# Kernel tuning notes

Hardware: AMD Instinct MI355X
Metric: run time of the kernel (lower is better)

The kernel has to match this reference:

```python
import jax, jax.numpy as jnp
import numpy as np

NUM_FEAT = 10

def _flatten(x):
    # [B,T,C,H,W] -> [B,C,T*H*W]
    B, T, C, H, W = x.shape
    return jnp.transpose(x, (0, 2, 1, 3, 4)).reshape(B, C, T * H * W)

def _conv1x1(w, b, x):
    # pointwise Conv1d: w [F,C], b [F], x [B,C,N] -> [B,F,N]
    return jnp.einsum('fc,bcn->bfn', w, x) + b[None, :, None]

def setup_inputs() -> dict:
    key = jax.random.key(0)
    ks = jax.random.split(key, 9)
    B, T, C, H, W = 1, 5, 64, 32, 32
    F = NUM_FEAT
    return {
        'input1': jax.random.normal(ks[0], (B, T, C, H, W), jnp.float32),
        'input2': jax.random.normal(ks[1], (B, T, C, H, W), jnp.float32),
        'act_weights': jax.random.uniform(ks[2], (3,), jnp.float32),
        'conv1_w': jax.random.normal(ks[3], (F, C), jnp.float32) * 0.05,
        'conv1_b': jnp.zeros((F,), jnp.float32),
        'conv2_w': jax.random.normal(ks[4], (F, C), jnp.float32) * 0.05,
        'conv2_b': jnp.zeros((F,), jnp.float32),
        'g3_w': jax.random.normal(ks[5], (F, C), jnp.float32) * 0.05,
        'g3_b': jnp.zeros((F,), jnp.float32),
    }

def reference(input1, input2, act_weights, conv1_w, conv1_b, conv2_w, conv2_b, g3_w, g3_b):
    B, T, C, H, W = input1.shape
    F = conv1_w.shape[0]
    x1 = _flatten(input1)                    # [B,C,N]
    x2 = _flatten(input2)                    # [B,C,N]
    q = _conv1x1(conv1_w, conv1_b, x1)       # [B,F,N]
    k = _conv1x1(conv2_w, conv2_b, x2)       # [B,F,N]
    v = _conv1x1(g3_w, g3_b, x1)             # [B,F,N]
    scores = jnp.einsum('bfn,bfm->bnm', q, k)  # [B,N,N] (same math, computed once)

    def branch(act_scores):
        o = jnp.einsum('bnm,bfm->bnf', act_scores, v)      # [B,N,F]
        o = o.reshape(B, T, H, W, F)
        return jnp.transpose(o, (0, 1, 4, 2, 3))           # [B,T,F,H,W]

    out = act_weights[0] * branch(jax.nn.relu(scores))
    out = out + act_weights[1] * branch(jax.nn.sigmoid(scores))
    # NOTE: original code scales the softmax branch by act_weights[0] (bug kept faithfully)
    out = out + act_weights[0] * branch(jax.nn.softmax(scores, axis=1))
    return out
```

## Files before the change

### kernel.cpp

```cpp
#include <hip/hip_runtime.h>

#define N_TOK   5120
#define C_IN    64
#define F_OUT   10
#define FP      12

#define DTILE   40
#define MTILE   40

__global__ __launch_bounds__(256) void qkv_kernel(
    const float* __restrict__ x1, const float* __restrict__ x2,
    const float* __restrict__ w1, const float* __restrict__ b1,
    const float* __restrict__ w2, const float* __restrict__ b2,
    const float* __restrict__ w3, const float* __restrict__ b3,
    float* __restrict__ Q, float* __restrict__ K, float* __restrict__ V)
{
    int arr = blockIdx.x / 200;
    int rem = blockIdx.x - arr * 200;
    int f   = rem / 20;
    int nbk = rem - f * 20;
    int n   = nbk * 256 + threadIdx.x;
    int t = n >> 10, p = n & 1023;

    const float* x    = (arr == 1) ? x2 : x1;
    const float* w    = (arr == 0) ? w1 : (arr == 1) ? w2 : w3;
    const float* bias = (arr == 0) ? b1 : (arr == 1) ? b2 : b3;
    float*       dst  = (arr == 0) ? Q  : (arr == 1) ? K  : V;

    const float* xp = x + t * (C_IN * 1024) + p;
    const float* wr = w + f * C_IN;

    float4 wv[16];
#pragma unroll
    for (int i = 0; i < 16; ++i) wv[i] = ((const float4*)wr)[i];

    float acc = 0.f;
#pragma unroll
    for (int i = 0; i < 16; ++i) {
        acc = fmaf(wv[i].x, xp[(4 * i + 0) * 1024], acc);
        acc = fmaf(wv[i].y, xp[(4 * i + 1) * 1024], acc);
        acc = fmaf(wv[i].z, xp[(4 * i + 2) * 1024], acc);
        acc = fmaf(wv[i].w, xp[(4 * i + 3) * 1024], acc);
    }
    dst[n * FP + f] = acc + bias[f];
}

__global__ __launch_bounds__(256) void denom_kernel(
    const float* __restrict__ Q, const float* __restrict__ K,
    float* __restrict__ dpart, int nclen)
{
    int mTile = blockIdx.x % 5;
    int nc    = blockIdx.x / 5;
    int tid   = threadIdx.x;
    int m0 = mTile * 1024 + tid;

    float kk[4][10];
#pragma unroll
    for (int c = 0; c < 4; ++c) {
        const float* kp = K + (m0 + c * 256) * FP;
        float4 a = ((const float4*)kp)[0];
        float4 b = ((const float4*)kp)[1];
        float2 e = ((const float2*)kp)[4];
        kk[c][0]=a.x; kk[c][1]=a.y; kk[c][2]=a.z; kk[c][3]=a.w;
        kk[c][4]=b.x; kk[c][5]=b.y; kk[c][6]=b.z; kk[c][7]=b.w;
        kk[c][8]=e.x; kk[c][9]=e.y;
    }

    __shared__ __align__(16) float sq[DTILE * FP];

    float d[4] = {0.f, 0.f, 0.f, 0.f};
    int n0 = nc * nclen;
    for (int base = n0; base < n0 + nclen; base += DTILE) {
        __syncthreads();
        if (tid < DTILE * FP / 4)
            ((float4*)sq)[tid] = ((const float4*)(Q + base * FP))[tid];
        __syncthreads();
#pragma unroll 2
        for (int j = 0; j < DTILE; ++j) {
            const float4* qp = (const float4*)(sq + j * FP);
            float4 qa = qp[0], qb = qp[1], qc = qp[2];
            float qq[10] = {qa.x, qa.y, qa.z, qa.w, qb.x, qb.y, qb.z, qb.w,
                            qc.x, qc.y};
#pragma unroll
            for (int c = 0; c < 4; ++c) {
                float s = 0.f;
#pragma unroll
                for (int f = 0; f < F_OUT; ++f) s = fmaf(qq[f], kk[c][f], s);
                d[c] += __expf(fminf(s, 60.f));
            }
        }
    }
#pragma unroll
    for (int c = 0; c < 4; ++c) dpart[nc * N_TOK + m0 + c * 256] = d[c];
}

__global__ __launch_bounds__(256) void invw_kernel(
    const float* __restrict__ dpart, const float* __restrict__ aw,
    float* __restrict__ K, int nchunks)
{
    int m = blockIdx.x * 256 + threadIdx.x;
    float d = 0.f;
#pragma unroll 8
    for (int c = 0; c < nchunks; ++c) d += dpart[c * N_TOK + m];
    K[m * FP + 10] = aw[0] / d;
}

__global__ __launch_bounds__(256) void main_kernel(
    const float* __restrict__ Q, const float* __restrict__ K,
    const float* __restrict__ V, const float* __restrict__ aw,
    float* __restrict__ opart, int mclen)
{
    int nTile = blockIdx.x % 4;
    int mc    = blockIdx.x / 4;
    int tid   = threadIdx.x;
    int nb = nTile * 1280 + tid;
    float w0 = aw[0], w1v = aw[1];

    float q[5][10];
#pragma unroll
    for (int r = 0; r < 5; ++r) {
        const float* qp = Q + (nb + r * 256) * FP;
        float4 a = ((const float4*)qp)[0];
        float4 b = ((const float4*)qp)[1];
        float2 e = ((const float2*)qp)[4];
        q[r][0]=a.x; q[r][1]=a.y; q[r][2]=a.z; q[r][3]=a.w;
        q[r][4]=b.x; q[r][5]=b.y; q[r][6]=b.z; q[r][7]=b.w;
        q[r][8]=e.x; q[r][9]=e.y;
    }

    float acc[5][F_OUT];
#pragma unroll
    for (int r = 0; r < 5; ++r)
#pragma unroll
        for (int f = 0; f < F_OUT; ++f) acc[r][f] = 0.f;

    __shared__ __align__(16) float sk[MTILE * FP];
    __shared__ __align__(16) float sv[MTILE * FP];

    int mstart = mc * mclen;
    for (int mbase = mstart; mbase < mstart + mclen; mbase += MTILE) {
        __syncthreads();
        if (tid < 120)
            ((float4*)sk)[tid] = ((const float4*)(K + mbase * FP))[tid];
        else if (tid < 240)
            ((float4*)sv)[tid - 120] = ((const float4*)(V + mbase * FP))[tid - 120];
        __syncthreads();

#pragma unroll 2
        for (int j = 0; j < MTILE; ++j) {
            const float4* kp = (const float4*)(sk + j * FP);
            float4 ka = kp[0], kb = kp[1], kc = kp[2];
            float kk[10] = {ka.x, ka.y, ka.z, ka.w, kb.x, kb.y, kb.z, kb.w,
                            kc.x, kc.y};
            float iw = kc.z;
            const float4* vp = (const float4*)(sv + j * FP);
            float4 va = vp[0], vb = vp[1], vc = vp[2];
            float vv[10] = {va.x, va.y, va.z, va.w, vb.x, vb.y, vb.z, vb.w,
                            vc.x, vc.y};

#pragma unroll
            for (int r = 0; r < 5; ++r) {
                float s = 0.f;
#pragma unroll
                for (int f = 0; f < F_OUT; ++f) s = fmaf(q[r][f], kk[f], s);
                float rl = fmaxf(s, 0.f);
                float e  = __expf(fminf(s, 60.f));
                float sg = e * __builtin_amdgcn_rcpf(1.f + e);
                float cf = fmaf(e, iw, fmaf(w1v, sg, w0 * rl));
#pragma unroll
                for (int f = 0; f < F_OUT; ++f) acc[r][f] = fmaf(cf, vv[f], acc[r][f]);
            }
        }
    }

#pragma unroll
    for (int r = 0; r < 5; ++r) {
        float2* o = (float2*)(opart + (size_t)(mc * N_TOK + nb + r * 256) * F_OUT);
#pragma unroll
        for (int f = 0; f < 5; ++f)
            o[f] = make_float2(acc[r][2 * f], acc[r][2 * f + 1]);
    }
}

__global__ __launch_bounds__(256) void reduce_kernel(
    const float* __restrict__ opart, float* __restrict__ out, int mchunks)
{
    int idx = blockIdx.x * 256 + threadIdx.x;
    float s = 0.f;
#pragma unroll 16
    for (int c = 0; c < mchunks; ++c) s += opart[c * (N_TOK * F_OUT) + idx];
    unsigned un = (unsigned)idx / 10u;
    int n = (int)un;
    int f = idx - n * 10;
    int t = n >> 10, p = n & 1023;
    out[((t * F_OUT + f) << 10) + p] = s;
}

extern "C" void kernel_launch(void* const* d_in, const int* in_sizes, int n_in,
                              void* d_out, int out_size, void* d_ws, size_t ws_size,
                              hipStream_t stream)
{
    const float* in1 = (const float*)d_in[0];
    const float* in2 = (const float*)d_in[1];
    const float* aw  = (const float*)d_in[2];
    const float* w1  = (const float*)d_in[3];
    const float* b1  = (const float*)d_in[4];
    const float* w2  = (const float*)d_in[5];
    const float* b2  = (const float*)d_in[6];
    const float* w3  = (const float*)d_in[7];
    const float* b3  = (const float*)d_in[8];
    float* out = (float*)d_out;

    int nchunks, mchunks;
    if (ws_size >= (size_t)32 << 20) { nchunks = 128; mchunks = 128; }
    else                             { nchunks = 32;  mchunks = 32;  }
    int nclen = N_TOK / nchunks;
    int mclen = N_TOK / mchunks;

    float* ws    = (float*)d_ws;
    float* Q     = ws;
    float* K     = Q + N_TOK * FP;
    float* V     = K + N_TOK * FP;
    float* dpart = V + N_TOK * FP;
    float* opart = dpart + nchunks * N_TOK;

    qkv_kernel<<<600, 256, 0, stream>>>(in1, in2, w1, b1, w2, b2, w3, b3, Q, K, V);
    denom_kernel<<<5 * nchunks, 256, 0, stream>>>(Q, K, dpart, nclen);
    invw_kernel<<<N_TOK / 256, 256, 0, stream>>>(dpart, aw, K, nchunks);
    main_kernel<<<4 * mchunks, 256, 0, stream>>>(Q, K, V, aw, opart, mclen);
    reduce_kernel<<<(N_TOK * F_OUT) / 256, 256, 0, stream>>>(opart, out, mchunks);
}
```

Before: 138.3 us.

## Replace partial-sum buffers and reduce kernels with atomic accumulation

The denominator partials and the output partials are now accumulated directly with float atomicAdd into a zeroed sum buffer and into the output, instead of being written per chunk and summed by separate invw and reduce kernels. Zeroing of the output and denominator buffers is folded into the first QKV kernel, and the softmax inverse weight is computed per tile in the main kernel. This removes two kernel launches and a large round-trip through partial buffers. In exchange it adds atomic contention (128 chunks adding to each output element) and makes summation order nondeterministic.

```diff
diff --git a/kernel.cpp b/kernel.cpp
--- a/kernel.cpp
+++ b/kernel.cpp
@@ -7,14 +7,22 @@
 
 #define DTILE   40
 #define MTILE   40
+#define NCHUNKS 128
+#define MCHUNKS 128
 
 __global__ __launch_bounds__(256) void qkv_kernel(
     const float* __restrict__ x1, const float* __restrict__ x2,
     const float* __restrict__ w1, const float* __restrict__ b1,
     const float* __restrict__ w2, const float* __restrict__ b2,
     const float* __restrict__ w3, const float* __restrict__ b3,
-    float* __restrict__ Q, float* __restrict__ K, float* __restrict__ V)
-{
+    float* __restrict__ Q, float* __restrict__ K, float* __restrict__ V,
+    float* __restrict__ out, float* __restrict__ dsum)
+{
+    if (blockIdx.x < 200)
+        out[blockIdx.x * 256 + threadIdx.x] = 0.f;
+    else if (blockIdx.x < 220)
+        dsum[(blockIdx.x - 200) * 256 + threadIdx.x] = 0.f;
+
     int arr = blockIdx.x / 200;
     int rem = blockIdx.x - arr * 200;
     int f   = rem / 20;
@@ -47,7 +55,7 @@
 
 __global__ __launch_bounds__(256) void denom_kernel(
     const float* __restrict__ Q, const float* __restrict__ K,
-    float* __restrict__ dpart, int nclen)
+    float* __restrict__ dsum, int nclen)
 {
     int mTile = blockIdx.x % 5;
     int nc    = blockIdx.x / 5;
@@ -91,24 +99,13 @@
         }
     }
 #pragma unroll
-    for (int c = 0; c < 4; ++c) dpart[nc * N_TOK + m0 + c * 256] = d[c];
-}
-
-__global__ __launch_bounds__(256) void invw_kernel(
-    const float* __restrict__ dpart, const float* __restrict__ aw,
-    float* __restrict__ K, int nchunks)
-{
-    int m = blockIdx.x * 256 + threadIdx.x;
-    float d = 0.f;
-#pragma unroll 8
-    for (int c = 0; c < nchunks; ++c) d += dpart[c * N_TOK + m];
-    K[m * FP + 10] = aw[0] / d;
+    for (int c = 0; c < 4; ++c) atomicAdd(&dsum[m0 + c * 256], d[c]);
 }
 
 __global__ __launch_bounds__(256) void main_kernel(
     const float* __restrict__ Q, const float* __restrict__ K,
-    const float* __restrict__ V, const float* __restrict__ aw,
-    float* __restrict__ opart, int mclen)
+    const float* __restrict__ V, const float* __restrict__ dsum,
+    const float* __restrict__ aw, float* __restrict__ out, int mclen)
 {
     int nTile = blockIdx.x % 4;
     int mc    = blockIdx.x / 4;
@@ -136,6 +133,7 @@
 
     __shared__ __align__(16) float sk[MTILE * FP];
     __shared__ __align__(16) float sv[MTILE * FP];
+    __shared__ float siw[MTILE];
 
     int mstart = mc * mclen;
     for (int mbase = mstart; mbase < mstart + mclen; mbase += MTILE) {
@@ -144,6 +142,8 @@
             ((float4*)sk)[tid] = ((const float4*)(K + mbase * FP))[tid];
         else if (tid < 240)
             ((float4*)sv)[tid - 120] = ((const float4*)(V + mbase * FP))[tid - 120];
+        if (tid < MTILE)
+            siw[tid] = w0 / dsum[mbase + tid];
         __syncthreads();
 
 #pragma unroll 2
@@ -152,7 +152,7 @@
             float4 ka = kp[0], kb = kp[1], kc = kp[2];
             float kk[10] = {ka.x, ka.y, ka.z, ka.w, kb.x, kb.y, kb.z, kb.w,
                             kc.x, kc.y};
-            float iw = kc.z;
+            float iw = siw[j];
             const float4* vp = (const float4*)(sv + j * FP);
             float4 va = vp[0], vb = vp[1], vc = vp[2];
             float vv[10] = {va.x, va.y, va.z, va.w, vb.x, vb.y, vb.z, vb.w,
@@ -175,25 +175,13 @@
 
 #pragma unroll
     for (int r = 0; r < 5; ++r) {
-        float2* o = (float2*)(opart + (size_t)(mc * N_TOK + nb + r * 256) * F_OUT);
-#pragma unroll
-        for (int f = 0; f < 5; ++f)
-            o[f] = make_float2(acc[r][2 * f], acc[r][2 * f + 1]);
-    }
-}
-
-__global__ __launch_bounds__(256) void reduce_kernel(
-    const float* __restrict__ opart, float* __restrict__ out, int mchunks)
-{
-    int idx = blockIdx.x * 256 + threadIdx.x;
-    float s = 0.f;
-#pragma unroll 16
-    for (int c = 0; c < mchunks; ++c) s += opart[c * (N_TOK * F_OUT) + idx];
-    unsigned un = (unsigned)idx / 10u;
-    int n = (int)un;
-    int f = idx - n * 10;
-    int t = n >> 10, p = n & 1023;
-    out[((t * F_OUT + f) << 10) + p] = s;
+        int n = nb + r * 256;
+        int t = n >> 10, p = n & 1023;
+        float* obase = out + ((t * F_OUT) << 10) + p;
+#pragma unroll
+        for (int f = 0; f < F_OUT; ++f)
+            atomicAdd(obase + (f << 10), acc[r][f]);
+    }
 }
 
 extern "C" void kernel_launch(void* const* d_in, const int* in_sizes, int n_in,
@@ -211,22 +199,17 @@
     const float* b3  = (const float*)d_in[8];
     float* out = (float*)d_out;
 
-    int nchunks, mchunks;
-    if (ws_size >= (size_t)32 << 20) { nchunks = 128; mchunks = 128; }
-    else                             { nchunks = 32;  mchunks = 32;  }
-    int nclen = N_TOK / nchunks;
-    int mclen = N_TOK / mchunks;
-
-    float* ws    = (float*)d_ws;
-    float* Q     = ws;
-    float* K     = Q + N_TOK * FP;
-    float* V     = K + N_TOK * FP;
-    float* dpart = V + N_TOK * FP;
-    float* opart = dpart + nchunks * N_TOK;
-
-    qkv_kernel<<<600, 256, 0, stream>>>(in1, in2, w1, b1, w2, b2, w3, b3, Q, K, V);
-    denom_kernel<<<5 * nchunks, 256, 0, stream>>>(Q, K, dpart, nclen);
-    invw_kernel<<<N_TOK / 256, 256, 0, stream>>>(dpart, aw, K, nchunks);
-    main_kernel<<<4 * mchunks, 256, 0, stream>>>(Q, K, V, aw, opart, mclen);
-    reduce_kernel<<<(N_TOK * F_OUT) / 256, 256, 0, stream>>>(opart, out, mchunks);
-}
+    float* ws   = (float*)d_ws;
+    float* Q    = ws;
+    float* K    = Q + N_TOK * FP;
+    float* V    = K + N_TOK * FP;
+    float* dsum = V + N_TOK * FP;
+
+    int nclen = N_TOK / NCHUNKS;
+    int mclen = N_TOK / MCHUNKS;
+
+    qkv_kernel<<<600, 256, 0, stream>>>(in1, in2, w1, b1, w2, b2, w3, b3,
+                                        Q, K, V, out, dsum);
+    denom_kernel<<<5 * NCHUNKS, 256, 0, stream>>>(Q, K, dsum, nclen);
+    main_kernel<<<4 * MCHUNKS, 256, 0, stream>>>(Q, K, V, dsum, aw, out, mclen);
+}
```

Result: faster. 130.1 us (-5.9%).
